# Kernel tuning notes

Measured on AMD Instinct MI355X. Metric: run time of the kernel, lower is better.

Reference implementation:

```python
import jax, jax.numpy as jnp
import numpy as np

B, S, D, H = 512, 512, 64, 128  # batch, seq_len, input_size, hidden_size


def setup_inputs() -> dict:
    key = jax.random.key(0)
    ks = jax.random.split(key, 12)
    s_in = 1.0 / np.sqrt(H)
    def u(k, shape):
        return jax.random.uniform(k, shape, jnp.float32, -s_in, s_in)
    return {
        "x": jax.random.normal(ks[0], (B, S, D), jnp.float32),
        # layer 0 (PyTorch gate order i,f,g,o stacked along first dim)
        "W_ih0": u(ks[1], (4 * H, D)),
        "W_hh0": u(ks[2], (4 * H, H)),
        "b_ih0": u(ks[3], (4 * H,)),
        "b_hh0": u(ks[4], (4 * H,)),
        # layer 1
        "W_ih1": u(ks[5], (4 * H, H)),
        "W_hh1": u(ks[6], (4 * H, H)),
        "b_ih1": u(ks[7], (4 * H,)),
        "b_hh1": u(ks[8], (4 * H,)),
        # linear head hidden -> 1
        "W_lin": u(ks[9], (1, H)),
        "b_lin": u(ks[10], (1,)),
    }


def _lstm_layer(x, W_ih, W_hh, b_ih, b_hh):
    # x: [B, S, Din] -> h sequence [B, S, H]
    b, s, _ = x.shape
    h_dim = W_hh.shape[1]
    # precompute input contribution for all timesteps (the compute-heavy GEMM)
    pre = jnp.einsum('bsd,gd->bsg', x, W_ih) + (b_ih + b_hh)  # [B, S, 4H]

    def step(carry, p_t):
        h, c = carry
        gates = p_t + h @ W_hh.T  # [B, 4H]
        i, f, g, o = jnp.split(gates, 4, axis=-1)
        i = jax.nn.sigmoid(i)
        f = jax.nn.sigmoid(f)
        g = jnp.tanh(g)
        o = jax.nn.sigmoid(o)
        c = f * c + i * g
        h = o * jnp.tanh(c)
        return (h, c), h

    h0 = jnp.zeros((b, h_dim), x.dtype)
    (_, _), hs = jax.lax.scan(step, (h0, h0), pre.transpose(1, 0, 2))
    return hs.transpose(1, 0, 2)  # [B, S, H]


def reference(x, W_ih0, W_hh0, b_ih0, b_hh0, W_ih1, W_hh1, b_ih1, b_hh1, W_lin, b_lin):
    h1 = _lstm_layer(x, W_ih0, W_hh0, b_ih0, b_hh0)
    h2 = _lstm_layer(h1, W_ih1, W_hh1, b_ih1, b_hh1)
    last = h2[:, -1, :]  # [B, H]
    return last @ W_lin.T + b_lin  # [B, 1]
```

## Files before the change

### kernel.cpp

```cpp
#include <hip/hip_runtime.h>

typedef _Float16 half8 __attribute__((ext_vector_type(8)));
typedef _Float16 half4 __attribute__((ext_vector_type(4)));
typedef _Float16 half2v __attribute__((ext_vector_type(2)));
typedef float floatx4 __attribute__((ext_vector_type(4)));

__device__ __forceinline__ float fast_rcp(float x) { return __builtin_amdgcn_rcpf(x); }
__device__ __forceinline__ float fast_sigmoid(float x) {
  return fast_rcp(1.f + __expf(-x));
}
__device__ __forceinline__ float fast_tanh(float x) {
  return 1.f - 2.f * fast_rcp(1.f + __expf(2.f * x));
}

__global__ void prep_kernel(const float* __restrict__ wih0, const float* __restrict__ whh0,
                            const float* __restrict__ bih0, const float* __restrict__ bhh0,
                            const float* __restrict__ wih1, const float* __restrict__ whh1,
                            const float* __restrict__ bih1, const float* __restrict__ bhh1,
                            _Float16* __restrict__ w0f, _Float16* __restrict__ w1f,
                            float* __restrict__ bias0, float* __restrict__ bias1)
{
  int stride = gridDim.x * blockDim.x;
  int idx0 = blockIdx.x * blockDim.x + threadIdx.x;
  const int N0 = 6*32*64*8;
  const int N1 = 8*32*64*8;
  for (int e = idx0; e < N0 + N1 + 1024; e += stride) {
    if (e < N0) {
      int j = e & 7; int le = e >> 3; int lane = le & 63; int frag = le >> 6;
      int kt = frag >> 5, ntile = frag & 31;
      int n = ntile*16 + (lane & 15);
      int kk = kt*32 + ((lane >> 4) << 3) + j;
      float v = (kk < 64) ? wih0[n*64 + kk] : whh0[n*128 + (kk - 64)];
      w0f[e] = (_Float16)v;
    } else if (e < N0 + N1) {
      int e2 = e - N0;
      int j = e2 & 7; int le = e2 >> 3; int lane = le & 63; int frag = le >> 6;
      int kt = frag >> 5, ntile = frag & 31;
      int n = ntile*16 + (lane & 15);
      int kk = kt*32 + ((lane >> 4) << 3) + j;
      float v = (kk < 128) ? wih1[n*128 + kk] : whh1[n*128 + (kk - 128)];
      w1f[e2] = (_Float16)v;
    } else {
      int i = e - (N0 + N1);
      if (i < 512) bias0[i] = bih0[i] + bhh0[i];
      else         bias1[i - 512] = bih1[i - 512] + bhh1[i - 512];
    }
  }
}


__global__ __launch_bounds__(512, 2) void lstm_l0(const float* __restrict__ x,
    const _Float16* __restrict__ w0f, const float* __restrict__ bias0,
    _Float16* __restrict__ h1out)
{
  const int tid = threadIdx.x;
  const int lane = tid & 63;
  const int w = tid >> 6;
  const int r0 = blockIdx.x * 2;

  __shared__ float preLDS[2][8192];
  __shared__ half8 aF[2][2*64];
  __shared__ half8 hA[2][4*8];
  __shared__ _Float16 hist[16][2][128];

  for (int i = tid; i < 2*4*8*4; i += 512) ((int*)hA)[i] = 0;

  half8 bf[6][4];
#pragma unroll
  for (int kt = 0; kt < 6; ++kt)
#pragma unroll
    for (int g = 0; g < 4; ++g) {
      int frag = kt*32 + (g*8 + w);
      bf[kt][g] = *reinterpret_cast<const half8*>(w0f + (size_t)(frag*64 + lane)*8);
      asm volatile("" : "+a"(bf[kt][g]));
    }
  float bias_v[4];
#pragma unroll
  for (int g = 0; g < 4; ++g) bias_v[g] = bias0[g*128 + w*16 + (lane & 15)];

  const int sdt = tid >> 6, sr = (tid >> 5) & 1, scp = (tid & 31) * 2;
  const int sm = sdt*2 + sr;
  const int sidx = ((scp>>5)*64 + sm + (((scp&31)>>3)<<4))*8 + (scp & 7);

  const bool arow = (lane & 11) == 0;
  const int cIdx = ((lane >> 4) << 1) | ((lane >> 2) & 1);
  const int rb = lane >> 4;
  const int en = w*16 + (lane & 15);
  const int eoff = ((en>>5)*8 + ((en&31)>>3)*2 + rb)*8 + (en&7);
  float cst = 0.f;

  {
    float2 v0 = *reinterpret_cast<const float2*>(x + ((size_t)(r0+sr)*512 + sdt)*64 + scp);
    float2 v1 = *reinterpret_cast<const float2*>(x + ((size_t)(r0+sr)*512 + 8 + sdt)*64 + scp);
    half2v h0; h0[0] = (_Float16)v0.x; h0[1] = (_Float16)v0.y;
    half2v h1v; h1v[0] = (_Float16)v1.x; h1v[1] = (_Float16)v1.y;
    *reinterpret_cast<half2v*>(((_Float16*)aF[0]) + sidx) = h0;
    *reinterpret_cast<half2v*>(((_Float16*)aF[1]) + sidx) = h1v;
  }
  __syncthreads();
  {
    floatx4 accP[4];
#pragma unroll
    for (int g = 0; g < 4; ++g) { float bb = bias_v[g]; accP[g] = (floatx4){bb,bb,bb,bb}; }
#pragma unroll
    for (int kt = 0; kt < 2; ++kt) {
      half8 af = aF[0][kt*64 + lane];
#pragma unroll
      for (int g = 0; g < 4; ++g)
        accP[g] = __builtin_amdgcn_mfma_f32_16x16x32_f16(af, bf[kt][g], accP[g], 0, 0, 0);
    }
#pragma unroll
    for (int reg = 0; reg < 4; ++reg) {
      int m = ((lane>>4)<<2) + reg;
      floatx4 pv = (floatx4){accP[0][reg], accP[1][reg], accP[2][reg], accP[3][reg]};
      *reinterpret_cast<floatx4*>(&preLDS[0][(m*128 + en)*4]) = pv;
    }
  }
  __syncthreads();

  half8 a2 = {}, a3 = {}, a4 = {}, a5 = {};

  for (int t = 0; t < 512; ++t) {
    const int b = t >> 3;
    if ((t & 7) == 0 && b < 62) {
      int s = (b+2)*8 + sdt;
      float2 v = *reinterpret_cast<const float2*>(x + ((size_t)(r0+sr)*512 + s)*64 + scp);
      half2v hv; hv[0] = (_Float16)v.x; hv[1] = (_Float16)v.y;
      *reinterpret_cast<half2v*>(((_Float16*)aF[b&1]) + sidx) = hv;
    }
    __syncthreads();
    if ((t & 7) == 0) {
      if (t != 0) {
        int tbase = t - 8;
        int fr = tid >> 8, rest = tid & 255;
        int fdt = rest >> 5, n = (rest & 31) * 4;
        half4 v = *reinterpret_cast<const half4*>(&hist[(tbase + fdt) & 15][fr][n]);
        *reinterpret_cast<half4*>(h1out + ((size_t)(r0 + fr)*512 + tbase + fdt)*128 + n) = v;
      }
      if (b < 63) {
        int slot = (b+1) & 1;
        floatx4 accP[4];
#pragma unroll
        for (int g = 0; g < 4; ++g) { float bb = bias_v[g]; accP[g] = (floatx4){bb,bb,bb,bb}; }
#pragma unroll
        for (int kt = 0; kt < 2; ++kt) {
          half8 af = aF[slot][kt*64 + lane];
#pragma unroll
          for (int g = 0; g < 4; ++g)
            accP[g] = __builtin_amdgcn_mfma_f32_16x16x32_f16(af, bf[kt][g], accP[g], 0, 0, 0);
        }
#pragma unroll
        for (int reg = 0; reg < 4; ++reg) {
          int m = ((lane>>4)<<2) + reg;
          floatx4 pv = (floatx4){accP[0][reg], accP[1][reg], accP[2][reg], accP[3][reg]};
          *reinterpret_cast<floatx4*>(&preLDS[slot][(m*128 + en)*4]) = pv;
        }
      }
    }

    floatx4 p4 = (floatx4){0.f, 0.f, 0.f, 0.f};
    if (lane < 32) {
      int mstep = ((t & 7) << 1) + rb;
      p4 = *reinterpret_cast<const floatx4*>(&preLDS[b & 1][(mstep*128 + en)*4]);
    }
    floatx4 acc[4];
#pragma unroll
    for (int g = 0; g < 4; ++g) acc[g] = (floatx4){p4[g], 0.f, 0.f, 0.f};

    const int cur = t & 1;
    if (arow) {
      a2 = hA[cur][0*8 + cIdx];
      a3 = hA[cur][1*8 + cIdx];
      a4 = hA[cur][2*8 + cIdx];
      a5 = hA[cur][3*8 + cIdx];
    }
#pragma unroll
    for (int g = 0; g < 4; ++g)
      acc[g] = __builtin_amdgcn_mfma_f32_16x16x32_f16(a2, bf[2][g], acc[g], 0, 0, 0);
#pragma unroll
    for (int g = 0; g < 4; ++g)
      acc[g] = __builtin_amdgcn_mfma_f32_16x16x32_f16(a3, bf[3][g], acc[g], 0, 0, 0);
#pragma unroll
    for (int g = 0; g < 4; ++g)
      acc[g] = __builtin_amdgcn_mfma_f32_16x16x32_f16(a4, bf[4][g], acc[g], 0, 0, 0);
#pragma unroll
    for (int g = 0; g < 4; ++g)
      acc[g] = __builtin_amdgcn_mfma_f32_16x16x32_f16(a5, bf[5][g], acc[g], 0, 0, 0);

    if (lane < 32) {
      float ii = fast_sigmoid(acc[0][0]);
      float ff = fast_sigmoid(acc[1][0]);
      float gg = fast_tanh(acc[2][0]);
      float oo = fast_sigmoid(acc[3][0]);
      cst = ff*cst + ii*gg;
      float hv2 = oo*fast_tanh(cst);
      _Float16 hh = (_Float16)hv2;
      ((_Float16*)hA[cur^1])[eoff] = hh;
      hist[t & 15][rb][en] = hh;
    }
  }
  __syncthreads();
  {
    int tbase = 504;
    int fr = tid >> 8, rest = tid & 255;
    int fdt = rest >> 5, n = (rest & 31) * 4;
    half4 v = *reinterpret_cast<const half4*>(&hist[(tbase + fdt) & 15][fr][n]);
    *reinterpret_cast<half4*>(h1out + ((size_t)(r0 + fr)*512 + tbase + fdt)*128 + n) = v;
  }
}

__global__ __launch_bounds__(512, 2) void lstm_l1(const _Float16* __restrict__ h1in,
    const _Float16* __restrict__ w1f, const float* __restrict__ bias1,
    const float* __restrict__ wlin, const float* __restrict__ blin,
    float* __restrict__ out)
{
  const int tid = threadIdx.x;
  const int lane = tid & 63;
  const int w = tid >> 6;
  const int r0 = blockIdx.x * 2;

  __shared__ float preLDS[2][8192];
  __shared__ half8 aF[2][4*64];
  __shared__ half8 hA[2][4*8];
  __shared__ float head[256];

  for (int i = tid; i < 2*4*8*4; i += 512) ((int*)hA)[i] = 0;

  half8 bf[8][4];
#pragma unroll
  for (int kt = 0; kt < 8; ++kt)
#pragma unroll
    for (int g = 0; g < 4; ++g) {
      int frag = kt*32 + (g*8 + w);
      bf[kt][g] = *reinterpret_cast<const half8*>(w1f + (size_t)(frag*64 + lane)*8);
      asm volatile("" : "+a"(bf[kt][g]));
    }
  float bias_v[4];
#pragma unroll
  for (int g = 0; g < 4; ++g) bias_v[g] = bias1[g*128 + w*16 + (lane & 15)];

  const int sdt = tid >> 6, sr = (tid >> 5) & 1, scq = (tid & 31) * 4;
  const int sm = sdt*2 + sr;
  const int sidx = ((scq>>5)*64 + sm + (((scq&31)>>3)<<4))*8 + (scq & 7);

  const bool arow = (lane & 11) == 0;
  const int cIdx = ((lane >> 4) << 1) | ((lane >> 2) & 1);
  const int rb = lane >> 4;
  const int en = w*16 + (lane & 15);
  const int eoff = ((en>>5)*8 + ((en&31)>>3)*2 + rb)*8 + (en&7);
  const float wl = (lane < 32) ? wlin[en] : 0.f;
  float cst = 0.f;
  float hl = 0.f;

  {
    uint2 v0 = *reinterpret_cast<const uint2*>(h1in + ((size_t)(r0+sr)*512 + sdt)*128 + scq);
    uint2 v1 = *reinterpret_cast<const uint2*>(h1in + ((size_t)(r0+sr)*512 + 8 + sdt)*128 + scq);
    *reinterpret_cast<uint2*>(((_Float16*)aF[0]) + sidx) = v0;
    *reinterpret_cast<uint2*>(((_Float16*)aF[1]) + sidx) = v1;
  }
  __syncthreads();
  {
    floatx4 accP[4];
#pragma unroll
    for (int g = 0; g < 4; ++g) { float bb = bias_v[g]; accP[g] = (floatx4){bb,bb,bb,bb}; }
#pragma unroll
    for (int kt = 0; kt < 4; ++kt) {
      half8 af = aF[0][kt*64 + lane];
#pragma unroll
      for (int g = 0; g < 4; ++g)
        accP[g] = __builtin_amdgcn_mfma_f32_16x16x32_f16(af, bf[kt][g], accP[g], 0, 0, 0);
    }
#pragma unroll
    for (int reg = 0; reg < 4; ++reg) {
      int m = ((lane>>4)<<2) + reg;
      floatx4 pv = (floatx4){accP[0][reg], accP[1][reg], accP[2][reg], accP[3][reg]};
      *reinterpret_cast<floatx4*>(&preLDS[0][(m*128 + en)*4]) = pv;
    }
  }
  __syncthreads();

  half8 a4 = {}, a5 = {}, a6 = {}, a7 = {};

  for (int t = 0; t < 512; ++t) {
    const int b = t >> 3;
    if ((t & 7) == 0 && b < 62) {
      int s = (b+2)*8 + sdt;
      uint2 v = *reinterpret_cast<const uint2*>(h1in + ((size_t)(r0+sr)*512 + s)*128 + scq);
      *reinterpret_cast<uint2*>(((_Float16*)aF[b&1]) + sidx) = v;
    }
    __syncthreads();
    if ((t & 7) == 0 && b < 63) {
      int slot = (b+1) & 1;
      floatx4 accP[4];
#pragma unroll
      for (int g = 0; g < 4; ++g) { float bb = bias_v[g]; accP[g] = (floatx4){bb,bb,bb,bb}; }
#pragma unroll
      for (int kt = 0; kt < 4; ++kt) {
        half8 af = aF[slot][kt*64 + lane];
#pragma unroll
        for (int g = 0; g < 4; ++g)
          accP[g] = __builtin_amdgcn_mfma_f32_16x16x32_f16(af, bf[kt][g], accP[g], 0, 0, 0);
      }
#pragma unroll
      for (int reg = 0; reg < 4; ++reg) {
        int m = ((lane>>4)<<2) + reg;
        floatx4 pv = (floatx4){accP[0][reg], accP[1][reg], accP[2][reg], accP[3][reg]};
        *reinterpret_cast<floatx4*>(&preLDS[slot][(m*128 + en)*4]) = pv;
      }
    }

    floatx4 p4 = (floatx4){0.f, 0.f, 0.f, 0.f};
    if (lane < 32) {
      int mstep = ((t & 7) << 1) + rb;
      p4 = *reinterpret_cast<const floatx4*>(&preLDS[b & 1][(mstep*128 + en)*4]);
    }
    floatx4 acc[4];
#pragma unroll
    for (int g = 0; g < 4; ++g) acc[g] = (floatx4){p4[g], 0.f, 0.f, 0.f};

    const int cur = t & 1;
    if (arow) {
      a4 = hA[cur][0*8 + cIdx];
      a5 = hA[cur][1*8 + cIdx];
      a6 = hA[cur][2*8 + cIdx];
      a7 = hA[cur][3*8 + cIdx];
    }
#pragma unroll
    for (int g = 0; g < 4; ++g)
      acc[g] = __builtin_amdgcn_mfma_f32_16x16x32_f16(a4, bf[4][g], acc[g], 0, 0, 0);
#pragma unroll
    for (int g = 0; g < 4; ++g)
      acc[g] = __builtin_amdgcn_mfma_f32_16x16x32_f16(a5, bf[5][g], acc[g], 0, 0, 0);
#pragma unroll
    for (int g = 0; g < 4; ++g)
      acc[g] = __builtin_amdgcn_mfma_f32_16x16x32_f16(a6, bf[6][g], acc[g], 0, 0, 0);
#pragma unroll
    for (int g = 0; g < 4; ++g)
      acc[g] = __builtin_amdgcn_mfma_f32_16x16x32_f16(a7, bf[7][g], acc[g], 0, 0, 0);

    if (lane < 32) {
      float ii = fast_sigmoid(acc[0][0]);
      float ff = fast_sigmoid(acc[1][0]);
      float gg = fast_tanh(acc[2][0]);
      float oo = fast_sigmoid(acc[3][0]);
      cst = ff*cst + ii*gg;
      hl = oo*fast_tanh(cst);
      ((_Float16*)hA[cur^1])[eoff] = (_Float16)hl;
    }
  }

  if (lane < 32) head[rb*128 + en] = hl * wl;
  __syncthreads();
  if (tid < 2) {
    float s = blin[0];
    for (int n = 0; n < 128; ++n) s += head[tid*128 + n];
    out[r0 + tid] = s;
  }
}

extern "C" void kernel_launch(void* const* d_in, const int* in_sizes, int n_in,
                              void* d_out, int out_size, void* d_ws, size_t ws_size,
                              hipStream_t stream)
{
  const float* x    = (const float*)d_in[0];
  const float* wih0 = (const float*)d_in[1];
  const float* whh0 = (const float*)d_in[2];
  const float* bih0 = (const float*)d_in[3];
  const float* bhh0 = (const float*)d_in[4];
  const float* wih1 = (const float*)d_in[5];
  const float* whh1 = (const float*)d_in[6];
  const float* bih1 = (const float*)d_in[7];
  const float* bhh1 = (const float*)d_in[8];
  const float* wlin = (const float*)d_in[9];
  const float* blin = (const float*)d_in[10];
  float* out = (float*)d_out;

  char* ws = (char*)d_ws;
  _Float16* w0f = (_Float16*)(ws);
  _Float16* w1f = (_Float16*)(ws + 196608);
  float* bias0  = (float*)(ws + 458752);
  float* bias1  = (float*)(ws + 460800);
  _Float16* h1  = (_Float16*)(ws + 1048576);

  prep_kernel<<<256, 256, 0, stream>>>(wih0, whh0, bih0, bhh0, wih1, whh1, bih1, bhh1,
                                       w0f, w1f, bias0, bias1);
  lstm_l0<<<256, 512, 0, stream>>>(x, w0f, bias0, h1);
  lstm_l1<<<256, 512, 0, stream>>>(h1, w1f, bias1, wlin, blin, out);
}
```

Baseline: 782.4 us.

## Fuse both LSTM layers into one cooperative kernel with progress-flag pipelining

Replaces the two sequential layer kernels with one cooperative launch. Blocks 0-127 run layer 0 and blocks 128-255 run layer 1 concurrently. Layer-1 blocks spin on per-pair progress counters that layer-0 blocks publish with release stores after writing h1 chunks to global memory. Each block now handles 4 batch rows instead of 2, using all 64 lanes of the 16-row MFMA tile rather than half. The aim is to overlap the two serial recurrences instead of running them back to back. The cost is spin-wait polling and the risk of deadlock if not all blocks are co-resident.

```diff
diff --git a/kernel.cpp b/kernel.cpp
--- a/kernel.cpp
+++ b/kernel.cpp
@@ -1,7 +1,6 @@
 #include <hip/hip_runtime.h>
 
 typedef _Float16 half8 __attribute__((ext_vector_type(8)));
-typedef _Float16 half4 __attribute__((ext_vector_type(4)));
 typedef _Float16 half2v __attribute__((ext_vector_type(2)));
 typedef float floatx4 __attribute__((ext_vector_type(4)));
 
@@ -18,13 +17,14 @@
                             const float* __restrict__ wih1, const float* __restrict__ whh1,
                             const float* __restrict__ bih1, const float* __restrict__ bhh1,
                             _Float16* __restrict__ w0f, _Float16* __restrict__ w1f,
-                            float* __restrict__ bias0, float* __restrict__ bias1)
+                            float* __restrict__ bias0, float* __restrict__ bias1,
+                            int* __restrict__ prog)
 {
   int stride = gridDim.x * blockDim.x;
   int idx0 = blockIdx.x * blockDim.x + threadIdx.x;
   const int N0 = 6*32*64*8;
   const int N1 = 8*32*64*8;
-  for (int e = idx0; e < N0 + N1 + 1024; e += stride) {
+  for (int e = idx0; e < N0 + N1 + 1024 + 128; e += stride) {
     if (e < N0) {
       int j = e & 7; int le = e >> 3; int lane = le & 63; int frag = le >> 6;
       int kt = frag >> 5, ntile = frag & 31;
@@ -40,321 +40,316 @@
       int kk = kt*32 + ((lane >> 4) << 3) + j;
       float v = (kk < 128) ? wih1[n*128 + kk] : whh1[n*128 + (kk - 128)];
       w1f[e2] = (_Float16)v;
-    } else {
+    } else if (e < N0 + N1 + 1024) {
       int i = e - (N0 + N1);
       if (i < 512) bias0[i] = bih0[i] + bhh0[i];
       else         bias1[i - 512] = bih1[i - 512] + bhh1[i - 512];
+    } else {
+      prog[e - (N0 + N1 + 1024)] = 0;
     }
   }
 }
 
 
-__global__ __launch_bounds__(512, 2) void lstm_l0(const float* __restrict__ x,
+__global__ __launch_bounds__(512, 2) void lstm_fused(
+    const float* __restrict__ x,
     const _Float16* __restrict__ w0f, const float* __restrict__ bias0,
-    _Float16* __restrict__ h1out)
+    const _Float16* __restrict__ w1f, const float* __restrict__ bias1,
+    const float* __restrict__ wlin, const float* __restrict__ blin,
+    _Float16* __restrict__ h1buf, int* __restrict__ prog,
+    float* __restrict__ out)
 {
+  __shared__ __align__(16) char smem[88064];
   const int tid = threadIdx.x;
   const int lane = tid & 63;
   const int w = tid >> 6;
-  const int r0 = blockIdx.x * 2;
-
-  __shared__ float preLDS[2][8192];
-  __shared__ half8 aF[2][2*64];
-  __shared__ half8 hA[2][4*8];
-  __shared__ _Float16 hist[16][2][128];
-
-  for (int i = tid; i < 2*4*8*4; i += 512) ((int*)hA)[i] = 0;
-
-  half8 bf[6][4];
-#pragma unroll
-  for (int kt = 0; kt < 6; ++kt)
-#pragma unroll
-    for (int g = 0; g < 4; ++g) {
-      int frag = kt*32 + (g*8 + w);
-      bf[kt][g] = *reinterpret_cast<const half8*>(w0f + (size_t)(frag*64 + lane)*8);
-      asm volatile("" : "+a"(bf[kt][g]));
-    }
-  float bias_v[4];
-#pragma unroll
-  for (int g = 0; g < 4; ++g) bias_v[g] = bias0[g*128 + w*16 + (lane & 15)];
-
-  const int sdt = tid >> 6, sr = (tid >> 5) & 1, scp = (tid & 31) * 2;
-  const int sm = sdt*2 + sr;
-  const int sidx = ((scp>>5)*64 + sm + (((scp&31)>>3)<<4))*8 + (scp & 7);
-
-  const bool arow = (lane & 11) == 0;
-  const int cIdx = ((lane >> 4) << 1) | ((lane >> 2) & 1);
+
+  const int sdt = tid >> 7, sr2 = (tid >> 5) & 3;
+  const bool arow = (lane & 3) == 0;
+  const int cIdx = (lane >> 4)*4 + ((lane >> 2) & 3);
   const int rb = lane >> 4;
   const int en = w*16 + (lane & 15);
-  const int eoff = ((en>>5)*8 + ((en&31)>>3)*2 + rb)*8 + (en&7);
-  float cst = 0.f;
-
-  {
-    float2 v0 = *reinterpret_cast<const float2*>(x + ((size_t)(r0+sr)*512 + sdt)*64 + scp);
-    float2 v1 = *reinterpret_cast<const float2*>(x + ((size_t)(r0+sr)*512 + 8 + sdt)*64 + scp);
-    half2v h0; h0[0] = (_Float16)v0.x; h0[1] = (_Float16)v0.y;
-    half2v h1v; h1v[0] = (_Float16)v1.x; h1v[1] = (_Float16)v1.y;
-    *reinterpret_cast<half2v*>(((_Float16*)aF[0]) + sidx) = h0;
-    *reinterpret_cast<half2v*>(((_Float16*)aF[1]) + sidx) = h1v;
-  }
-  __syncthreads();
-  {
-    floatx4 accP[4];
-#pragma unroll
-    for (int g = 0; g < 4; ++g) { float bb = bias_v[g]; accP[g] = (floatx4){bb,bb,bb,bb}; }
-#pragma unroll
-    for (int kt = 0; kt < 2; ++kt) {
-      half8 af = aF[0][kt*64 + lane];
-#pragma unroll
-      for (int g = 0; g < 4; ++g)
-        accP[g] = __builtin_amdgcn_mfma_f32_16x16x32_f16(af, bf[kt][g], accP[g], 0, 0, 0);
-    }
-#pragma unroll
-    for (int reg = 0; reg < 4; ++reg) {
-      int m = ((lane>>4)<<2) + reg;
-      floatx4 pv = (floatx4){accP[0][reg], accP[1][reg], accP[2][reg], accP[3][reg]};
-      *reinterpret_cast<floatx4*>(&preLDS[0][(m*128 + en)*4]) = pv;
-    }
-  }
-  __syncthreads();
-
-  half8 a2 = {}, a3 = {}, a4 = {}, a5 = {};
-
-  for (int t = 0; t < 512; ++t) {
-    const int b = t >> 3;
-    if ((t & 7) == 0 && b < 62) {
-      int s = (b+2)*8 + sdt;
-      float2 v = *reinterpret_cast<const float2*>(x + ((size_t)(r0+sr)*512 + s)*64 + scp);
+  const int eoff = ((en>>5)*16 + ((en&31)>>3)*4 + rb)*8 + (en&7);
+
+  if (blockIdx.x < 128) {
+    const int pair = blockIdx.x;
+    const int r0 = pair * 4;
+    float* preLDS  = (float*)smem;
+    half8* aF      = (half8*)(smem + 65536);
+    half8* hA      = (half8*)(smem + 69632);
+    _Float16* hist = (_Float16*)(smem + 71680);
+
+    for (int i = tid; i < 512; i += 512) ((int*)hA)[i] = 0;
+
+    half8 bf[6][4];
+#pragma unroll
+    for (int kt = 0; kt < 6; ++kt)
+#pragma unroll
+      for (int g = 0; g < 4; ++g) {
+        int frag = kt*32 + (g*8 + w);
+        bf[kt][g] = *reinterpret_cast<const half8*>(w0f + (size_t)(frag*64 + lane)*8);
+        asm volatile("" : "+a"(bf[kt][g]));
+      }
+    float bias_v[4];
+#pragma unroll
+    for (int g = 0; g < 4; ++g) bias_v[g] = bias0[g*128 + w*16 + (lane & 15)];
+
+    const int scp = (tid & 31) * 2;
+    const int sm = sdt*4 + sr2;
+    const int sidx = ((scp>>5)*64 + sm + (((scp&31)>>3)<<4))*8 + (scp & 7);
+    float cst = 0.f;
+
+#pragma unroll
+    for (int bb = 0; bb < 2; ++bb) {
+      float2 v = *reinterpret_cast<const float2*>(x + ((size_t)(r0+sr2)*512 + bb*4 + sdt)*64 + scp);
       half2v hv; hv[0] = (_Float16)v.x; hv[1] = (_Float16)v.y;
-      *reinterpret_cast<half2v*>(((_Float16*)aF[b&1]) + sidx) = hv;
-    }
-    __syncthreads();
-    if ((t & 7) == 0) {
-      if (t != 0) {
-        int tbase = t - 8;
-        int fr = tid >> 8, rest = tid & 255;
-        int fdt = rest >> 5, n = (rest & 31) * 4;
-        half4 v = *reinterpret_cast<const half4*>(&hist[(tbase + fdt) & 15][fr][n]);
-        *reinterpret_cast<half4*>(h1out + ((size_t)(r0 + fr)*512 + tbase + fdt)*128 + n) = v;
-      }
-      if (b < 63) {
+      *reinterpret_cast<half2v*>(((_Float16*)(aF + bb*128)) + sidx) = hv;
+    }
+    __syncthreads();
+    {
+      floatx4 accP[4];
+#pragma unroll
+      for (int g = 0; g < 4; ++g) { float bb = bias_v[g]; accP[g] = (floatx4){bb,bb,bb,bb}; }
+#pragma unroll
+      for (int kt = 0; kt < 2; ++kt) {
+        half8 af = aF[0*128 + kt*64 + lane];
+#pragma unroll
+        for (int g = 0; g < 4; ++g)
+          accP[g] = __builtin_amdgcn_mfma_f32_16x16x32_f16(af, bf[kt][g], accP[g], 0, 0, 0);
+      }
+#pragma unroll
+      for (int reg = 0; reg < 4; ++reg) {
+        int m = (lane>>4)*4 + reg;
+        floatx4 pv = (floatx4){accP[0][reg], accP[1][reg], accP[2][reg], accP[3][reg]};
+        *reinterpret_cast<floatx4*>(&preLDS[(m*128 + en)*4]) = pv;
+      }
+    }
+    __syncthreads();
+
+    half8 a2 = {}, a3 = {}, a4 = {}, a5 = {};
+
+    for (int t = 0; t < 512; ++t) {
+      const int b = t >> 2;
+      if ((t & 3) == 0 && b < 126) {
+        int s = (b+2)*4 + sdt;
+        float2 v = *reinterpret_cast<const float2*>(x + ((size_t)(r0+sr2)*512 + s)*64 + scp);
+        half2v hv; hv[0] = (_Float16)v.x; hv[1] = (_Float16)v.y;
+        *reinterpret_cast<half2v*>(((_Float16*)(aF + (b&1)*128)) + sidx) = hv;
+      }
+      __syncthreads();
+      if ((t & 7) == 1 && t >= 9 && tid == 0)
+        __hip_atomic_store(&prog[pair], (t-1) >> 3, __ATOMIC_RELEASE, __HIP_MEMORY_SCOPE_AGENT);
+      if ((t & 3) == 0) {
+        if ((t & 7) == 0 && t != 0) {
+          int tbase = t - 8;
+          int fdt = tid >> 6, fr = (tid >> 4) & 3, n = (tid & 15) * 8;
+          half8 v = *reinterpret_cast<const half8*>(&hist[(((tbase+fdt)&15)*4 + fr)*128 + n]);
+          *reinterpret_cast<half8*>(h1buf + ((size_t)(r0+fr)*512 + tbase+fdt)*128 + n) = v;
+          __threadfence();
+        }
+        if (b < 127) {
+          int slot = (b+1) & 1;
+          floatx4 accP[4];
+#pragma unroll
+          for (int g = 0; g < 4; ++g) { float bb = bias_v[g]; accP[g] = (floatx4){bb,bb,bb,bb}; }
+#pragma unroll
+          for (int kt = 0; kt < 2; ++kt) {
+            half8 af = aF[slot*128 + kt*64 + lane];
+#pragma unroll
+            for (int g = 0; g < 4; ++g)
+              accP[g] = __builtin_amdgcn_mfma_f32_16x16x32_f16(af, bf[kt][g], accP[g], 0, 0, 0);
+          }
+#pragma unroll
+          for (int reg = 0; reg < 4; ++reg) {
+            int m = (lane>>4)*4 + reg;
+            floatx4 pv = (floatx4){accP[0][reg], accP[1][reg], accP[2][reg], accP[3][reg]};
+            *reinterpret_cast<floatx4*>(&preLDS[slot*8192 + (m*128 + en)*4]) = pv;
+          }
+        }
+      }
+
+      floatx4 p4 = *reinterpret_cast<const floatx4*>(
+          &preLDS[(b&1)*8192 + (((t&3)*4 + rb)*128 + en)*4]);
+      floatx4 acc[4];
+#pragma unroll
+      for (int g = 0; g < 4; ++g) acc[g] = (floatx4){p4[g], 0.f, 0.f, 0.f};
+
+      const int cur = t & 1;
+      if (arow) {
+        a2 = hA[cur*64 + 0*16 + cIdx];
+        a3 = hA[cur*64 + 1*16 + cIdx];
+        a4 = hA[cur*64 + 2*16 + cIdx];
+        a5 = hA[cur*64 + 3*16 + cIdx];
+      }
+#pragma unroll
+      for (int g = 0; g < 4; ++g)
+        acc[g] = __builtin_amdgcn_mfma_f32_16x16x32_f16(a2, bf[2][g], acc[g], 0, 0, 0);
+#pragma unroll
+      for (int g = 0; g < 4; ++g)
+        acc[g] = __builtin_amdgcn_mfma_f32_16x16x32_f16(a3, bf[3][g], acc[g], 0, 0, 0);
+#pragma unroll
+      for (int g = 0; g < 4; ++g)
+        acc[g] = __builtin_amdgcn_mfma_f32_16x16x32_f16(a4, bf[4][g], acc[g], 0, 0, 0);
+#pragma unroll
+      for (int g = 0; g < 4; ++g)
+        acc[g] = __builtin_amdgcn_mfma_f32_16x16x32_f16(a5, bf[5][g], acc[g], 0, 0, 0);
+
+      {
+        float ii = fast_sigmoid(acc[0][0]);
+        float ff = fast_sigmoid(acc[1][0]);
+        float gg = fast_tanh(acc[2][0]);
+        float oo = fast_sigmoid(acc[3][0]);
+        cst = ff*cst + ii*gg;
+        float hv2 = oo*fast_tanh(cst);
+        _Float16 hh = (_Float16)hv2;
+        ((_Float16*)hA)[(cur^1)*512 + eoff] = hh;
+        hist[((t&15)*4 + rb)*128 + en] = hh;
+      }
+    }
+    __syncthreads();
+    {
+      int tbase = 504;
+      int fdt = tid >> 6, fr = (tid >> 4) & 3, n = (tid & 15) * 8;
+      half8 v = *reinterpret_cast<const half8*>(&hist[(((tbase+fdt)&15)*4 + fr)*128 + n]);
+      *reinterpret_cast<half8*>(h1buf + ((size_t)(r0+fr)*512 + tbase+fdt)*128 + n) = v;
+      __threadfence();
+    }
+    __syncthreads();
+    if (tid == 0)
+      __hip_atomic_store(&prog[pair], 64, __ATOMIC_RELEASE, __HIP_MEMORY_SCOPE_AGENT);
+
+  } else {
+    const int pair = blockIdx.x - 128;
+    const int r0 = pair * 4;
+    float* preLDS = (float*)smem;
+    half8* aF     = (half8*)(smem + 65536);
+    half8* hA     = (half8*)(smem + 73728);
+    float* head   = (float*)(smem + 75776);
+
+    for (int i = tid; i < 512; i += 512) ((int*)hA)[i] = 0;
+
+    half8 bf[8][4];
+#pragma unroll
+    for (int kt = 0; kt < 8; ++kt)
+#pragma unroll
+      for (int g = 0; g < 4; ++g) {
+        int frag = kt*32 + (g*8 + w);
+        bf[kt][g] = *reinterpret_cast<const half8*>(w1f + (size_t)(frag*64 + lane)*8);
+        asm volatile("" : "+a"(bf[kt][g]));
+      }
+    float bias_v[4];
+#pragma unroll
+    for (int g = 0; g < 4; ++g) bias_v[g] = bias1[g*128 + w*16 + (lane & 15)];
+
+    const int scq = (tid & 31) * 4;
+    const int sm = sdt*4 + sr2;
+    const int sidx = ((scq>>5)*64 + sm + (((scq&31)>>3)<<4))*8 + (scq & 7);
+    const float wl = wlin[en];
+    float cst = 0.f, hl = 0.f;
+
+    while (__hip_atomic_load(&prog[pair], __ATOMIC_ACQUIRE, __HIP_MEMORY_SCOPE_AGENT) < 1) {}
+#pragma unroll
+    for (int bb = 0; bb < 2; ++bb) {
+      uint2 v = *reinterpret_cast<const uint2*>(h1buf + ((size_t)(r0+sr2)*512 + bb*4 + sdt)*128 + scq);
+      *reinterpret_cast<uint2*>(((_Float16*)(aF + bb*256)) + sidx) = v;
+    }
+    __syncthreads();
+    {
+      floatx4 accP[4];
+#pragma unroll
+      for (int g = 0; g < 4; ++g) { float bb = bias_v[g]; accP[g] = (floatx4){bb,bb,bb,bb}; }
+#pragma unroll
+      for (int kt = 0; kt < 4; ++kt) {
+        half8 af = aF[0*256 + kt*64 + lane];
+#pragma unroll
+        for (int g = 0; g < 4; ++g)
+          accP[g] = __builtin_amdgcn_mfma_f32_16x16x32_f16(af, bf[kt][g], accP[g], 0, 0, 0);
+      }
+#pragma unroll
+      for (int reg = 0; reg < 4; ++reg) {
+        int m = (lane>>4)*4 + reg;
+        floatx4 pv = (floatx4){accP[0][reg], accP[1][reg], accP[2][reg], accP[3][reg]};
+        *reinterpret_cast<floatx4*>(&preLDS[(m*128 + en)*4]) = pv;
+      }
+    }
+    __syncthreads();
+
+    half8 a4 = {}, a5 = {}, a6 = {}, a7 = {};
+
+    for (int t = 0; t < 512; ++t) {
+      const int b = t >> 2;
+      if ((t & 3) == 0 && b < 126) {
+        int need = (b + 4) >> 1;
+        while (__hip_atomic_load(&prog[pair], __ATOMIC_ACQUIRE, __HIP_MEMORY_SCOPE_AGENT) < need) {}
+        int s = (b+2)*4 + sdt;
+        uint2 v = *reinterpret_cast<const uint2*>(h1buf + ((size_t)(r0+sr2)*512 + s)*128 + scq);
+        *reinterpret_cast<uint2*>(((_Float16*)(aF + (b&1)*256)) + sidx) = v;
+      }
+      __syncthreads();
+      if ((t & 3) == 0 && b < 127) {
         int slot = (b+1) & 1;
         floatx4 accP[4];
 #pragma unroll
         for (int g = 0; g < 4; ++g) { float bb = bias_v[g]; accP[g] = (floatx4){bb,bb,bb,bb}; }
 #pragma unroll
-        for (int kt = 0; kt < 2; ++kt) {
-          half8 af = aF[slot][kt*64 + lane];
+        for (int kt = 0; kt < 4; ++kt) {
+          half8 af = aF[slot*256 + kt*64 + lane];
 #pragma unroll
           for (int g = 0; g < 4; ++g)
             accP[g] = __builtin_amdgcn_mfma_f32_16x16x32_f16(af, bf[kt][g], accP[g], 0, 0, 0);
         }
 #pragma unroll
         for (int reg = 0; reg < 4; ++reg) {
-          int m = ((lane>>4)<<2) + reg;
+          int m = (lane>>4)*4 + reg;
           floatx4 pv = (floatx4){accP[0][reg], accP[1][reg], accP[2][reg], accP[3][reg]};
-          *reinterpret_cast<floatx4*>(&preLDS[slot][(m*128 + en)*4]) = pv;
+          *reinterpret_cast<floatx4*>(&preLDS[slot*8192 + (m*128 + en)*4]) = pv;
         }
       }
-    }
-
-    floatx4 p4 = (floatx4){0.f, 0.f, 0.f, 0.f};
-    if (lane < 32) {
-      int mstep = ((t & 7) << 1) + rb;
-      p4 = *reinterpret_cast<const floatx4*>(&preLDS[b & 1][(mstep*128 + en)*4]);
-    }
-    floatx4 acc[4];
-#pragma unroll
-    for (int g = 0; g < 4; ++g) acc[g] = (floatx4){p4[g], 0.f, 0.f, 0.f};
-
-    const int cur = t & 1;
-    if (arow) {
-      a2 = hA[cur][0*8 + cIdx];
-      a3 = hA[cur][1*8 + cIdx];
-      a4 = hA[cur][2*8 + cIdx];
-      a5 = hA[cur][3*8 + cIdx];
-    }
-#pragma unroll
-    for (int g = 0; g < 4; ++g)
-      acc[g] = __builtin_amdgcn_mfma_f32_16x16x32_f16(a2, bf[2][g], acc[g], 0, 0, 0);
-#pragma unroll
-    for (int g = 0; g < 4; ++g)
-      acc[g] = __builtin_amdgcn_mfma_f32_16x16x32_f16(a3, bf[3][g], acc[g], 0, 0, 0);
-#pragma unroll
-    for (int g = 0; g < 4; ++g)
-      acc[g] = __builtin_amdgcn_mfma_f32_16x16x32_f16(a4, bf[4][g], acc[g], 0, 0, 0);
-#pragma unroll
-    for (int g = 0; g < 4; ++g)
-      acc[g] = __builtin_amdgcn_mfma_f32_16x16x32_f16(a5, bf[5][g], acc[g], 0, 0, 0);
-
-    if (lane < 32) {
-      float ii = fast_sigmoid(acc[0][0]);
-      float ff = fast_sigmoid(acc[1][0]);
-      float gg = fast_tanh(acc[2][0]);
-      float oo = fast_sigmoid(acc[3][0]);
-      cst = ff*cst + ii*gg;
-      float hv2 = oo*fast_tanh(cst);
-      _Float16 hh = (_Float16)hv2;
-      ((_Float16*)hA[cur^1])[eoff] = hh;
-      hist[t & 15][rb][en] = hh;
-    }
-  }
-  __syncthreads();
-  {
-    int tbase = 504;
-    int fr = tid >> 8, rest = tid & 255;
-    int fdt = rest >> 5, n = (rest & 31) * 4;
-    half4 v = *reinterpret_cast<const half4*>(&hist[(tbase + fdt) & 15][fr][n]);
-    *reinterpret_cast<half4*>(h1out + ((size_t)(r0 + fr)*512 + tbase + fdt)*128 + n) = v;
-  }
-}
-
-__global__ __launch_bounds__(512, 2) void lstm_l1(const _Float16* __restrict__ h1in,
-    const _Float16* __restrict__ w1f, const float* __restrict__ bias1,
-    const float* __restrict__ wlin, const float* __restrict__ blin,
-    float* __restrict__ out)
-{
-  const int tid = threadIdx.x;
-  const int lane = tid & 63;
-  const int w = tid >> 6;
-  const int r0 = blockIdx.x * 2;
-
-  __shared__ float preLDS[2][8192];
-  __shared__ half8 aF[2][4*64];
-  __shared__ half8 hA[2][4*8];
-  __shared__ float head[256];
-
-  for (int i = tid; i < 2*4*8*4; i += 512) ((int*)hA)[i] = 0;
-
-  half8 bf[8][4];
-#pragma unroll
-  for (int kt = 0; kt < 8; ++kt)
-#pragma unroll
-    for (int g = 0; g < 4; ++g) {
-      int frag = kt*32 + (g*8 + w);
-      bf[kt][g] = *reinterpret_cast<const half8*>(w1f + (size_t)(frag*64 + lane)*8);
-      asm volatile("" : "+a"(bf[kt][g]));
-    }
-  float bias_v[4];
-#pragma unroll
-  for (int g = 0; g < 4; ++g) bias_v[g] = bias1[g*128 + w*16 + (lane & 15)];
-
-  const int sdt = tid >> 6, sr = (tid >> 5) & 1, scq = (tid & 31) * 4;
-  const int sm = sdt*2 + sr;
-  const int sidx = ((scq>>5)*64 + sm + (((scq&31)>>3)<<4))*8 + (scq & 7);
-
-  const bool arow = (lane & 11) == 0;
-  const int cIdx = ((lane >> 4) << 1) | ((lane >> 2) & 1);
-  const int rb = lane >> 4;
-  const int en = w*16 + (lane & 15);
-  const int eoff = ((en>>5)*8 + ((en&31)>>3)*2 + rb)*8 + (en&7);
-  const float wl = (lane < 32) ? wlin[en] : 0.f;
-  float cst = 0.f;
-  float hl = 0.f;
-
-  {
-    uint2 v0 = *reinterpret_cast<const uint2*>(h1in + ((size_t)(r0+sr)*512 + sdt)*128 + scq);
-    uint2 v1 = *reinterpret_cast<const uint2*>(h1in + ((size_t)(r0+sr)*512 + 8 + sdt)*128 + scq);
-    *reinterpret_cast<uint2*>(((_Float16*)aF[0]) + sidx) = v0;
-    *reinterpret_cast<uint2*>(((_Float16*)aF[1]) + sidx) = v1;
-  }
-  __syncthreads();
-  {
-    floatx4 accP[4];
-#pragma unroll
-    for (int g = 0; g < 4; ++g) { float bb = bias_v[g]; accP[g] = (floatx4){bb,bb,bb,bb}; }
-#pragma unroll
-    for (int kt = 0; kt < 4; ++kt) {
-      half8 af = aF[0][kt*64 + lane];
-#pragma unroll
-      for (int g = 0; g < 4; ++g)
-        accP[g] = __builtin_amdgcn_mfma_f32_16x16x32_f16(af, bf[kt][g], accP[g], 0, 0, 0);
-    }
-#pragma unroll
-    for (int reg = 0; reg < 4; ++reg) {
-      int m = ((lane>>4)<<2) + reg;
-      floatx4 pv = (floatx4){accP[0][reg], accP[1][reg], accP[2][reg], accP[3][reg]};
-      *reinterpret_cast<floatx4*>(&preLDS[0][(m*128 + en)*4]) = pv;
-    }
-  }
-  __syncthreads();
-
-  half8 a4 = {}, a5 = {}, a6 = {}, a7 = {};
-
-  for (int t = 0; t < 512; ++t) {
-    const int b = t >> 3;
-    if ((t & 7) == 0 && b < 62) {
-      int s = (b+2)*8 + sdt;
-      uint2 v = *reinterpret_cast<const uint2*>(h1in + ((size_t)(r0+sr)*512 + s)*128 + scq);
-      *reinterpret_cast<uint2*>(((_Float16*)aF[b&1]) + sidx) = v;
-    }
-    __syncthreads();
-    if ((t & 7) == 0 && b < 63) {
-      int slot = (b+1) & 1;
-      floatx4 accP[4];
-#pragma unroll
-      for (int g = 0; g < 4; ++g) { float bb = bias_v[g]; accP[g] = (floatx4){bb,bb,bb,bb}; }
-#pragma unroll
-      for (int kt = 0; kt < 4; ++kt) {
-        half8 af = aF[slot][kt*64 + lane];
-#pragma unroll
-        for (int g = 0; g < 4; ++g)
-          accP[g] = __builtin_amdgcn_mfma_f32_16x16x32_f16(af, bf[kt][g], accP[g], 0, 0, 0);
-      }
-#pragma unroll
-      for (int reg = 0; reg < 4; ++reg) {
-        int m = ((lane>>4)<<2) + reg;
-        floatx4 pv = (floatx4){accP[0][reg], accP[1][reg], accP[2][reg], accP[3][reg]};
-        *reinterpret_cast<floatx4*>(&preLDS[slot][(m*128 + en)*4]) = pv;
-      }
-    }
-
-    floatx4 p4 = (floatx4){0.f, 0.f, 0.f, 0.f};
-    if (lane < 32) {
-      int mstep = ((t & 7) << 1) + rb;
-      p4 = *reinterpret_cast<const floatx4*>(&preLDS[b & 1][(mstep*128 + en)*4]);
-    }
-    floatx4 acc[4];
-#pragma unroll
-    for (int g = 0; g < 4; ++g) acc[g] = (floatx4){p4[g], 0.f, 0.f, 0.f};
-
-    const int cur = t & 1;
-    if (arow) {
-      a4 = hA[cur][0*8 + cIdx];
-      a5 = hA[cur][1*8 + cIdx];
-      a6 = hA[cur][2*8 + cIdx];
-      a7 = hA[cur][3*8 + cIdx];
-    }
-#pragma unroll
-    for (int g = 0; g < 4; ++g)
-      acc[g] = __builtin_amdgcn_mfma_f32_16x16x32_f16(a4, bf[4][g], acc[g], 0, 0, 0);
-#pragma unroll
-    for (int g = 0; g < 4; ++g)
-      acc[g] = __builtin_amdgcn_mfma_f32_16x16x32_f16(a5, bf[5][g], acc[g], 0, 0, 0);
-#pragma unroll
-    for (int g = 0; g < 4; ++g)
-      acc[g] = __builtin_amdgcn_mfma_f32_16x16x32_f16(a6, bf[6][g], acc[g], 0, 0, 0);
-#pragma unroll
-    for (int g = 0; g < 4; ++g)
-      acc[g] = __builtin_amdgcn_mfma_f32_16x16x32_f16(a7, bf[7][g], acc[g], 0, 0, 0);
-
-    if (lane < 32) {
-      float ii = fast_sigmoid(acc[0][0]);
-      float ff = fast_sigmoid(acc[1][0]);
-      float gg = fast_tanh(acc[2][0]);
-      float oo = fast_sigmoid(acc[3][0]);
-      cst = ff*cst + ii*gg;
-      hl = oo*fast_tanh(cst);
-      ((_Float16*)hA[cur^1])[eoff] = (_Float16)hl;
-    }
-  }
-
-  if (lane < 32) head[rb*128 + en] = hl * wl;
-  __syncthreads();
-  if (tid < 2) {
-    float s = blin[0];
-    for (int n = 0; n < 128; ++n) s += head[tid*128 + n];
-    out[r0 + tid] = s;
+
+      floatx4 p4 = *reinterpret_cast<const floatx4*>(
+          &preLDS[(b&1)*8192 + (((t&3)*4 + rb)*128 + en)*4]);
+      floatx4 acc[4];
+#pragma unroll
+      for (int g = 0; g < 4; ++g) acc[g] = (floatx4){p4[g], 0.f, 0.f, 0.f};
+
+      const int cur = t & 1;
+      if (arow) {
+        a4 = hA[cur*64 + 0*16 + cIdx];
+        a5 = hA[cur*64 + 1*16 + cIdx];
+        a6 = hA[cur*64 + 2*16 + cIdx];
+        a7 = hA[cur*64 + 3*16 + cIdx];
+      }
+#pragma unroll
+      for (int g = 0; g < 4; ++g)
+        acc[g] = __builtin_amdgcn_mfma_f32_16x16x32_f16(a4, bf[4][g], acc[g], 0, 0, 0);
+#pragma unroll
+      for (int g = 0; g < 4; ++g)
+        acc[g] = __builtin_amdgcn_mfma_f32_16x16x32_f16(a5, bf[5][g], acc[g], 0, 0, 0);
+#pragma unroll
+      for (int g = 0; g < 4; ++g)
+        acc[g] = __builtin_amdgcn_mfma_f32_16x16x32_f16(a6, bf[6][g], acc[g], 0, 0, 0);
+#pragma unroll
+      for (int g = 0; g < 4; ++g)
+        acc[g] = __builtin_amdgcn_mfma_f32_16x16x32_f16(a7, bf[7][g], acc[g], 0, 0, 0);
+
+      {
+        float ii = fast_sigmoid(acc[0][0]);
+        float ff = fast_sigmoid(acc[1][0]);
+        float gg = fast_tanh(acc[2][0]);
+        float oo = fast_sigmoid(acc[3][0]);
+        cst = ff*cst + ii*gg;
+        hl = oo*fast_tanh(cst);
+        ((_Float16*)hA)[(cur^1)*512 + eoff] = (_Float16)hl;
+      }
+    }
+
+    head[rb*128 + en] = hl * wl;
+    __syncthreads();
+    if (tid < 4) {
+      float s = blin[0];
+      for (int n = 0; n < 128; ++n) s += head[tid*128 + n];
+      out[r0 + tid] = s;
+    }
   }
 }
 
@@ -380,10 +375,13 @@
   _Float16* w1f = (_Float16*)(ws + 196608);
   float* bias0  = (float*)(ws + 458752);
   float* bias1  = (float*)(ws + 460800);
+  int* prog     = (int*)(ws + 462848);
   _Float16* h1  = (_Float16*)(ws + 1048576);
 
   prep_kernel<<<256, 256, 0, stream>>>(wih0, whh0, bih0, bhh0, wih1, whh1, bih1, bhh1,
-                                       w0f, w1f, bias0, bias1);
-  lstm_l0<<<256, 512, 0, stream>>>(x, w0f, bias0, h1);
-  lstm_l1<<<256, 512, 0, stream>>>(h1, w1f, bias1, wlin, blin, out);
-}
+                                       w0f, w1f, bias0, bias1, prog);
+
+  void* args[] = { (void*)&x, (void*)&w0f, (void*)&bias0, (void*)&w1f, (void*)&bias1,
+                   (void*)&wlin, (void*)&blin, (void*)&h1, (void*)&prog, (void*)&out };
+  hipLaunchCooperativeKernel((void*)lstm_fused, dim3(256), dim3(512), args, 0, stream);
+}
```

Measured after the change: 2.573 ms. 229% more time.
